# Optimization experiments

Measured on AMD Instinct MI355X. Metric: run time of the kernel, lower is better.

The kernel has to match this reference:

```python
import jax, jax.numpy as jnp
import numpy as np

C = 64        # channel_n
HID = 128     # hidden_size
HEADS = 4
HD = 16       # head_dim = embed_dim // heads, embed_dim overwritten to channel_n
INNER = HEADS * HD  # 64
MLP = 64
H = W = 64    # img_size
B = 8
STEPS = 6
IN_CH = 1     # input_channels
SCALE = HD ** -0.5


def conv3x3_reflect(x, w, b):
    # x: [B,C,H,W], w: [O,I,3,3] -- reflect padding like nn.Conv2d(padding_mode='reflect')
    xp = jnp.pad(x, ((0, 0), (0, 0), (1, 1), (1, 1)), mode='reflect')
    y = jax.lax.conv_general_dilated(xp, w, (1, 1), 'VALID',
                                     dimension_numbers=('NCHW', 'OIHW', 'NCHW'))
    return y + b[None, :, None, None]


def layernorm(x, w, b, axes):
    mu = jnp.mean(x, axis=axes, keepdims=True)
    var = jnp.var(x, axis=axes, keepdims=True)
    return (x - mu) * jax.lax.rsqrt(var + 1e-5) * w + b


def localize(t, h, w):
    # t: [B,heads,n,d] -> [B,heads,n,9,d]; zero-padded 3x3 neighbourhoods
    # (equivalent to grouped conv with 9 unit-impulse filters, padding='same')
    b, nh, n, d = t.shape
    g = t.reshape(b, nh, h, w, d)
    gp = jnp.pad(g, ((0, 0), (0, 0), (1, 1), (1, 1), (0, 0)))
    nb = jnp.stack([gp[:, :, i:i + h, j:j + w, :]
                    for i in range(3) for j in range(3)], axis=4)
    return nb.reshape(b, nh, n, 9, d)


def attn_block(t, ln_w, ln_b, qkv_w, out_w, out_b):
    y = layernorm(t, ln_w, ln_b, -1)
    qkv = y @ qkv_w.T                              # [B,n,3*inner]
    q, k, v = jnp.split(qkv, 3, axis=-1)
    to_heads = lambda z: z.reshape(z.shape[0], z.shape[1], HEADS, HD).transpose(0, 2, 1, 3)
    q, k, v = to_heads(q), to_heads(k), to_heads(v)   # [B,h,n,d]
    kl = localize(k, H, W)                          # [B,h,n,9,d]
    vl = localize(v, H, W)
    dots = jnp.einsum('bhnd,bhnkd->bhnk', q, kl) * SCALE
    a = jax.nn.softmax(dots, axis=-1)               # [B,h,n,9]
    o = jnp.einsum('bhnk,bhnkd->bhnd', a, vl)
    o = o.transpose(0, 2, 1, 3).reshape(t.shape[0], t.shape[1], INNER)
    return o @ out_w.T + out_b


def ff_block(t, ln_w, ln_b, w1, b1, w2, b2):
    y = layernorm(t, ln_w, ln_b, -1)
    y = jax.nn.gelu(y @ w1.T + b1, approximate=False)
    return y @ w2.T + b2


def setup_inputs() -> dict:
    key = jax.random.key(0)
    ks = jax.random.split(key, 20)
    s = 0.02
    inp = {
        'x': jax.random.normal(ks[0], (B, H, W, C), jnp.float32),
        'masks': jax.random.bernoulli(ks[1], 0.5, (STEPS, B, H, W, 1)),
        'p0_w': jax.random.normal(ks[2], (C, C, 3, 3)) * s,
        'p0_b': jnp.zeros((C,)),
        'p1_w': jax.random.normal(ks[3], (C, C, 3, 3)) * s,
        'p1_b': jnp.zeros((C,)),
        'fc0_w': jax.random.normal(ks[4], (HID, 3 * C)) * s,
        'fc0_b': jnp.zeros((HID,)),
        'fc1_w': jax.random.normal(ks[5], (C, HID)) * s,  # zero-init in torch; random here for a non-trivial test
        'norm0_w': jnp.ones((H, W, HID)),
        'norm0_b': jnp.zeros((H, W, HID)),
        'ln1_w': jnp.ones((C,)),
        'ln1_b': jnp.zeros((C,)),
        'qkv_w': jax.random.normal(ks[6], (3 * INNER, C)) * s,
        'out_w': jax.random.normal(ks[7], (C, INNER)) * s,
        'out_b': jnp.zeros((C,)),
        'ln2_w': jnp.ones((C,)),
        'ln2_b': jnp.zeros((C,)),
        'ff1_w': jax.random.normal(ks[8], (MLP, C)) * s,
        'ff1_b': jnp.zeros((MLP,)),
        'ff2_w': jax.random.normal(ks[9], (C, MLP)) * s,
        'ff2_b': jnp.zeros((C,)),
        'steps': STEPS,
    }
    return inp


def reference(x, masks, p0_w, p0_b, p1_w, p1_b, fc0_w, fc0_b, fc1_w,
              norm0_w, norm0_b, ln1_w, ln1_b, qkv_w, out_w, out_b,
              ln2_w, ln2_b, ff1_w, ff1_b, ff2_w, ff2_b, steps):
    def step(xc, mask):
        # ---- NCA perception + update (BackboneNCA.perceive + fc0/relu/norm/fc1) ----
        xt = xc.transpose(0, 3, 1, 2)                      # [B,C,H,W]
        y1 = conv3x3_reflect(xt, p0_w, p0_b)
        y2 = conv3x3_reflect(xt, p1_w, p1_b)
        p = jnp.concatenate([xt, y1, y2], 1).transpose(0, 2, 3, 1)  # [B,H,W,3C]
        hd = jax.nn.relu(p @ fc0_w.T + fc0_b)              # [B,H,W,HID]
        hd = layernorm(hd, norm0_w, norm0_b, (-3, -2, -1))  # norm0 over [H,W,HID]
        dx = hd @ fc1_w.T                                   # [B,H,W,C]
        dx = dx * mask.astype(xc.dtype)                     # stochastic fire
        xn = xc + dx
        # ---- ViT block with localized (3x3 windowed) attention ----
        t = xn.reshape(B, H * W, C)
        t = t + attn_block(t, ln1_w, ln1_b, qkv_w, out_w, out_b)
        t = t + ff_block(t, ln2_w, ln2_b, ff1_w, ff1_b, ff2_w, ff2_b)
        xn = t.reshape(B, H, W, C)
        # keep input channels unchanged
        xn = jnp.concatenate([xc[..., :IN_CH], xn[..., IN_CH:]], axis=-1)
        return xn, None

    out, _ = jax.lax.scan(step, x, masks)
    return out
```

## Files before the change

kernel.cpp:

```cpp
#include <hip/hip_runtime.h>
#include <hip/hip_bf16.h>

typedef __hip_bfloat16 bf16;
typedef __attribute__((ext_vector_type(8))) short bf16x8;
typedef __attribute__((ext_vector_type(4))) float f32x4;

#define NSTEP 6

static __device__ __forceinline__ float b2f(bf16 v) { return __bfloat162float(v); }

static __device__ __forceinline__ float ldp(const void* p, int i, int md) {
    return md ? ((const float*)p)[i] : b2f(((const bf16*)p)[i]);
}
static __device__ __forceinline__ float finz(float v) {
    return (v == v && v * 0.0f == 0.0f) ? v : 0.0f;
}
static __device__ __forceinline__ unsigned short f2bfu(float v) {
    bf16 h = __float2bfloat16(v);
    return *(unsigned short*)&h;
}

static __device__ __forceinline__ void ld_bf8(const bf16* p, float* f) {
    union { uint4 u; unsigned short s[8]; } r;
    r.u = *(const uint4*)p;
#pragma unroll
    for (int j = 0; j < 8; ++j) f[j] = __uint_as_float(((unsigned)r.s[j]) << 16);
}
static __device__ __forceinline__ void ldp8(const void* p, int i, int md, float* f) {
    if (md) {
        const float* fp = (const float*)p + i;
        float4 a = *(const float4*)fp, b = *(const float4*)(fp + 4);
        f[0]=a.x; f[1]=a.y; f[2]=a.z; f[3]=a.w; f[4]=b.x; f[5]=b.y; f[6]=b.z; f[7]=b.w;
    } else {
        ld_bf8((const bf16*)p + i, f);
    }
}
static __device__ __forceinline__ uint4 pk_bf8(const float* f) {
    union { uint4 u; unsigned short s[8]; } r;
#pragma unroll
    for (int j = 0; j < 8; ++j) r.s[j] = f2bfu(f[j]);
    return r.u;
}


__global__ void k_detect(const uint4* __restrict__ m4,
                         const uint4* __restrict__ x4,
                         int* __restrict__ flags, float* __restrict__ accv) {
    __shared__ int s3f, sup, slo, sf32;
    int t = threadIdx.x;
    if (t == 0) { s3f = 0; sup = 0; slo = 0; sf32 = 0; }
    if (t < 96) accv[t] = 0.f;
    __syncthreads();
    int l3f = 0, lup = 0, llo = 0, lf = 0;
    for (int i = t; i < 3072; i += 256) {
        uint4 v = m4[i];
        const unsigned* d = (const unsigned*)&v;
#pragma unroll
        for (int j = 0; j < 4; ++j) {
            unsigned w = d[j];
            unsigned x3f = w ^ 0x3F3F3F3Fu;
            if ((x3f - 0x01010101u) & ~x3f & 0x80808080u) l3f = 1;
            if (w & 0xFFFFFF00u) lup = 1;
            if (w & 0x0000FFFFu) llo = 1;
        }
    }
    for (int i = t; i < 4096; i += 256) {
        uint4 v = x4[i];
        const unsigned* d = (const unsigned*)&v;
#pragma unroll
        for (int j = 0; j < 4; ++j) {
            unsigned bb = (d[j] >> 8) & 0x7Fu;
            if (bb > 0x48u) lf = 1;
        }
    }
    if (l3f) atomicOr(&s3f, 1);
    if (lup) atomicOr(&sup, 1);
    if (llo) atomicOr(&slo, 1);
    if (lf)  atomicOr(&sf32, 1);
    __syncthreads();
    if (t == 0) {
        int mode;
        if (!s3f && !sup) mode = 0;
        else if (!s3f)    mode = 1;
        else if (slo)     mode = 2;
        else              mode = 3;
        flags[0] = mode;
        flags[1] = sf32;
    }
}

__global__ void k_cast(const void* __restrict__ in, float* __restrict__ out,
                       const int* __restrict__ mflags, int n8) {
    int md = mflags[1];
    int i = blockIdx.x * 256 + threadIdx.x;
    if (i < n8) {
        float f[8];
        ldp8(in, i * 8, md, f);
#pragma unroll
        for (int j = 0; j < 8; ++j) f[j] = finz(f[j]);
        *(float4*)&out[i * 8]     = make_float4(f[0], f[1], f[2], f[3]);
        *(float4*)&out[i * 8 + 4] = make_float4(f[4], f[5], f[6], f[7]);
    }
}

__global__ void k_pack_multi(const void* __restrict__ pa, const void* __restrict__ pb,
                             const void* __restrict__ pc, const void* __restrict__ pd,
                             const void* __restrict__ pe, const void* __restrict__ pf,
                             short* __restrict__ out, const int* __restrict__ mflags) {
    int md = mflags[1];
    int i = blockIdx.x * 256 + threadIdx.x;
    if (i >= 57344) return;
    float v;
    if      (i < 24576) v = ldp(pa, i, md);
    else if (i < 32768) v = ldp(pb, i - 24576, md);
    else if (i < 45056) v = ldp(pc, i - 32768, md);
    else if (i < 49152) v = ldp(pd, i - 45056, md);
    else if (i < 53248) v = ldp(pe, i - 49152, md);
    else                v = ldp(pf, i - 53248, md);
    out[i] = (short)f2bfu(v);
}

__global__ void k_pack_bt1(const void* __restrict__ p0, const void* __restrict__ p1,
                           short* __restrict__ out, const int* __restrict__ mflags) {
    int md = mflags[1];
    int i = blockIdx.x * 256 + threadIdx.x;
    if (i < 128 * 576) {
        int o = i / 576, k = i % 576;
        int kk = k >> 6, ii = k & 63;
        float v = (o < 64) ? ldp(p0, o * 576 + ii * 9 + kk, md)
                           : ldp(p1, (o - 64) * 576 + ii * 9 + kk, md);
        out[i] = (short)f2bfu(v);
    }
}

__global__ void k_fold(const void* __restrict__ n0w, const void* __restrict__ n0b,
                       const short* __restrict__ fc1s, float* __restrict__ wsum,
                       float* __restrict__ bconst, const int* __restrict__ mflags) {
    __shared__ short fc1T[128 * 64];
    int md = mflags[1];
    int t = threadIdx.x;
    for (int e = t; e < 8192; e += 256) {
        int c2 = e >> 7, j = e & 127;
        fc1T[j * 64 + c2] = fc1s[c2 * 128 + j];
    }
    __syncthreads();
    int c = t & 63, pl = t >> 6;
    int pos = blockIdx.x * 4 + pl;
    float ws = 0.f, bs = 0.f;
    for (int j = 0; j < 128; ++j) {
        float f = b2f(*(const bf16*)&fc1T[j * 64 + c]);
        ws = fmaf(ldp(n0w, pos * 128 + j, md), f, ws);
        bs = fmaf(ldp(n0b, pos * 128 + j, md), f, bs);
    }
    wsum[pos * 64 + c]   = ws;
    bconst[pos * 64 + c] = bs;
}


__global__ __launch_bounds__(512) void k_perceive(
    const float* __restrict__ xin, const short* __restrict__ bt1,
    const short* __restrict__ fc0s, const short* __restrict__ fc1s,
    const void* __restrict__ p0b, const void* __restrict__ p1b,
    const void* __restrict__ fc0b, const void* __restrict__ n0w,
    const int* __restrict__ mflags, float* __restrict__ t1,
    float* __restrict__ accv, int step)
{
    __shared__ __align__(16) short xpad_s[3 * 66 * 72];
    __shared__ __align__(16) short P_s[64 * 200];
    __shared__ __align__(16) short hd_s[64 * 136];
    __shared__ float red[32];
    int md = mflags[1];
    int bh = blockIdx.x;
    int b = bh >> 6, h = bh & 63;
    int t = threadIdx.x;

    for (int e = t; e < 1536; e += 512) {
        int c8 = e & 7, w = (e >> 3) & 63, r = e >> 9;
        int hr = h - 1 + r; hr = hr < 0 ? -hr : (hr > 63 ? 126 - hr : hr);
        const float* src = xin + ((((b << 6) + hr) << 6) | w) * 64 + c8 * 8;
        float f[8];
        float4 v0 = *(const float4*)src, v1 = *(const float4*)(src + 4);
        f[0]=v0.x; f[1]=v0.y; f[2]=v0.z; f[3]=v0.w; f[4]=v1.x; f[5]=v1.y; f[6]=v1.z; f[7]=v1.w;
        uint4 pv = pk_bf8(f);
        *(uint4*)&xpad_s[((r * 66) + w + 1) * 72 + c8 * 8] = pv;
        if (r == 1) *(uint4*)&P_s[w * 200 + c8 * 8] = pv;
    }
    if (t < 48) {
        int c8 = t & 7, side = (t >> 3) & 1, r = t >> 4;
        int hr = h - 1 + r; hr = hr < 0 ? -hr : (hr > 63 ? 126 - hr : hr);
        int wsrc = side ? 62 : 1, wp = side ? 65 : 0;
        const float* src = xin + ((((b << 6) + hr) << 6) | wsrc) * 64 + c8 * 8;
        float f[8];
        float4 v0 = *(const float4*)src, v1 = *(const float4*)(src + 4);
        f[0]=v0.x; f[1]=v0.y; f[2]=v0.z; f[3]=v0.w; f[4]=v1.x; f[5]=v1.y; f[6]=v1.z; f[7]=v1.w;
        *(uint4*)&xpad_s[((r * 66) + wp) * 72 + c8 * 8] = pk_bf8(f);
    }
    __syncthreads();

    int og  = __builtin_amdgcn_readfirstlane(t >> 6);
    int l   = t & 63, nl = l & 15, q = l >> 4;
    int mt0 = (og & 1) * 2;
    int nt0 = (og >> 1) * 2;
    int o0  = nt0 * 16 + nl, o1 = o0 + 16;

    f32x4 acc[2][2];
#pragma unroll
    for (int i = 0; i < 2; ++i)
#pragma unroll
        for (int j = 0; j < 2; ++j) acc[i][j] = (f32x4){0.f, 0.f, 0.f, 0.f};

    for (int kt = 0; kt < 18; ++kt) {
        int kk = kt >> 1, c0 = (kt & 1) << 5;
        int r = kk / 3, cxi = kk - r * 3;
        bf16x8 b0 = *(const bf16x8*)(bt1 + o0 * 576 + kt * 32 + q * 8);
        bf16x8 b1 = *(const bf16x8*)(bt1 + o1 * 576 + kt * 32 + q * 8);
        bf16x8 a0 = *(const bf16x8*)&xpad_s[((r * 66) + mt0 * 16 + nl + cxi) * 72 + c0 + q * 8];
        bf16x8 a1 = *(const bf16x8*)&xpad_s[((r * 66) + mt0 * 16 + 16 + nl + cxi) * 72 + c0 + q * 8];
        acc[0][0] = __builtin_amdgcn_mfma_f32_16x16x32_bf16(a0, b0, acc[0][0], 0, 0, 0);
        acc[0][1] = __builtin_amdgcn_mfma_f32_16x16x32_bf16(a0, b1, acc[0][1], 0, 0, 0);
        acc[1][0] = __builtin_amdgcn_mfma_f32_16x16x32_bf16(a1, b0, acc[1][0], 0, 0, 0);
        acc[1][1] = __builtin_amdgcn_mfma_f32_16x16x32_bf16(a1, b1, acc[1][1], 0, 0, 0);
    }
    {
        float bias0 = (o0 < 64) ? ldp(p0b, o0, md) : ldp(p1b, o0 - 64, md);
        float bias1 = (o1 < 64) ? ldp(p0b, o1, md) : ldp(p1b, o1 - 64, md);
#pragma unroll
        for (int i = 0; i < 2; ++i)
#pragma unroll
            for (int j = 0; j < 2; ++j) {
                int oo = j ? o1 : o0;
                float bb = j ? bias1 : bias0;
#pragma unroll
                for (int r2 = 0; r2 < 4; ++r2) {
                    int m = (mt0 + i) * 16 + q * 4 + r2;
                    P_s[m * 200 + 64 + oo] = (short)f2bfu(acc[i][j][r2] + bb);
                }
            }
    }
    __syncthreads();

#pragma unroll
    for (int i = 0; i < 2; ++i)
#pragma unroll
        for (int j = 0; j < 2; ++j) acc[i][j] = (f32x4){0.f, 0.f, 0.f, 0.f};
    for (int kt = 0; kt < 6; ++kt) {
        bf16x8 b0 = *(const bf16x8*)(fc0s + o0 * 192 + kt * 32 + q * 8);
        bf16x8 b1 = *(const bf16x8*)(fc0s + o1 * 192 + kt * 32 + q * 8);
        bf16x8 a0 = *(const bf16x8*)&P_s[(mt0 * 16 + nl) * 200 + kt * 32 + q * 8];
        bf16x8 a1 = *(const bf16x8*)&P_s[(mt0 * 16 + 16 + nl) * 200 + kt * 32 + q * 8];
        acc[0][0] = __builtin_amdgcn_mfma_f32_16x16x32_bf16(a0, b0, acc[0][0], 0, 0, 0);
        acc[0][1] = __builtin_amdgcn_mfma_f32_16x16x32_bf16(a0, b1, acc[0][1], 0, 0, 0);
        acc[1][0] = __builtin_amdgcn_mfma_f32_16x16x32_bf16(a1, b0, acc[1][0], 0, 0, 0);
        acc[1][1] = __builtin_amdgcn_mfma_f32_16x16x32_bf16(a1, b1, acc[1][1], 0, 0, 0);
    }
    float lsum = 0.f, lsq = 0.f;
    {
        float fb0 = ldp(fc0b, o0, md), fb1 = ldp(fc0b, o1, md);
#pragma unroll
        for (int i = 0; i < 2; ++i)
#pragma unroll
            for (int j = 0; j < 2; ++j) {
                int oo = j ? o1 : o0;
                float bb = j ? fb1 : fb0;
#pragma unroll
                for (int r2 = 0; r2 < 4; ++r2) {
                    int m = (mt0 + i) * 16 + q * 4 + r2;
                    float v = fmaxf(acc[i][j][r2] + bb, 0.f);
                    unsigned short hu = f2bfu(v);
                    hd_s[m * 136 + oo] = (short)hu;
                    float vr = __uint_as_float(((unsigned)hu) << 16);
                    lsum += vr; lsq += vr * vr;
                }
            }
    }
#pragma unroll
    for (int off = 32; off > 0; off >>= 1) {
        lsum += __shfl_down(lsum, off, 64);
        lsq  += __shfl_down(lsq,  off, 64);
    }
    if (l == 0) { red[og] = lsum; red[16 + og] = lsq; }
    __syncthreads();
    if (t == 0) {
        float a = 0.f, s2 = 0.f;
#pragma unroll
        for (int w = 0; w < 8; ++w) { a += red[w]; s2 += red[16 + w]; }
        atomicAdd(&accv[step * 16 + b * 2],     a);
        atomicAdd(&accv[step * 16 + b * 2 + 1], s2);
    }

    for (int e = t; e < 1024; e += 512) {
        int pos = e >> 4, j8 = (e & 15) * 8;
        float hv[8], wv[8];
        ld_bf8((const bf16*)&hd_s[pos * 136 + j8], hv);
        ldp8(n0w, (h * 64 + pos) * 128 + j8, md, wv);
#pragma unroll
        for (int j = 0; j < 8; ++j) hv[j] *= wv[j];
        *(uint4*)&hd_s[pos * 136 + j8] = pk_bf8(hv);
    }
    __syncthreads();

    {
        int mt = og & 3, nh = og >> 2;
        int to0 = nh * 32 + nl, to1 = to0 + 16;
        f32x4 a0 = (f32x4){0.f,0.f,0.f,0.f}, a1 = (f32x4){0.f,0.f,0.f,0.f};
#pragma unroll
        for (int kt = 0; kt < 4; ++kt) {
            bf16x8 av = *(const bf16x8*)&hd_s[(mt * 16 + nl) * 136 + kt * 32 + q * 8];
            bf16x8 b0 = *(const bf16x8*)(fc1s + to0 * 128 + kt * 32 + q * 8);
            bf16x8 b1 = *(const bf16x8*)(fc1s + to1 * 128 + kt * 32 + q * 8);
            a0 = __builtin_amdgcn_mfma_f32_16x16x32_bf16(av, b0, a0, 0, 0, 0);
            a1 = __builtin_amdgcn_mfma_f32_16x16x32_bf16(av, b1, a1, 0, 0, 0);
        }
#pragma unroll
        for (int r2 = 0; r2 < 4; ++r2) {
            int m = mt * 16 + q * 4 + r2;
            t1[((bh << 6) + m) * 64 + to0] = a0[r2];
            t1[((bh << 6) + m) * 64 + to1] = a1[r2];
        }
    }
}

__global__ __launch_bounds__(512) void k_step2(
    const float* __restrict__ xin, float* __restrict__ xout,
    const float* __restrict__ t1, const float* __restrict__ wsum,
    const float* __restrict__ bconst, const void* __restrict__ mraw,
    const short* __restrict__ qkvs, const void* __restrict__ ln1w,
    const void* __restrict__ ln1b, const short* __restrict__ outs,
    const short* __restrict__ ff1s, const short* __restrict__ ff2s,
    const void* __restrict__ outb, const void* __restrict__ ln2w,
    const void* __restrict__ ln2b, const void* __restrict__ ff1b,
    const void* __restrict__ ff2b, const int* __restrict__ mflags,
    const float* __restrict__ accv, void* __restrict__ dout,
    int step, int write_out)
{
    __shared__ __align__(16) char smraw[75456];
    short* Ks = (short*)smraw;
    short* Vs = (short*)(smraw + 28512);
    short* qo = (short*)(smraw + 57024);
    short* ys = (short*)(smraw + 66240);
    short* Ao = (short*)smraw;
    float* ts = (float*)(smraw + 9216);
    short* hs = (short*)(smraw + 25856);

    int md = mflags[1];
    int bh = blockIdx.x;
    int b = bh >> 6, h = bh & 63;
    int t = threadIdx.x;

    const float invN = 1.f / 524288.f;
    float mean = accv[step * 16 + b * 2] * invN;
    float var  = accv[step * 16 + b * 2 + 1] * invN - mean * mean;
    float rstd = rsqrtf(fmaxf(var, 0.f) + 1e-5f);
    float mrs  = mean * rstd;

    if (t < 96) {
        int kind = (t >= 48) ? 1 : 0, u = t - kind * 48;
        int r = u >> 4, side = (u >> 3) & 1, c8 = u & 7;
        short* dst = kind ? Vs : Ks;
        uint4 z = {0, 0, 0, 0};
        *(uint4*)&dst[((r * 66) + (side ? 65 : 0)) * 72 + c8 * 8] = z;
    }

    int og = __builtin_amdgcn_readfirstlane(t >> 6);
    int l = t & 63, nl = l & 15, q = l >> 4;
    int tok = t >> 3, j8 = (t & 7) * 8;
    int mmode = mflags[0];

    float tn[8];
    float c0 = 0.f;
#pragma unroll
    for (int ci = 0; ci < 8; ++ci) tn[ci] = 0.f;

    for (int r = 0; r < 3; ++r) {
        int hr = h - 1 + r;
        __syncthreads();
        if (hr < 0 || hr > 63) {
            for (int e = t; e < 1024; e += 512) {
                int kind = (e >= 512) ? 1 : 0, u = e & 511;
                int w = u >> 3, c8 = u & 7;
                short* dst = kind ? Vs : Ks;
                uint4 z = {0, 0, 0, 0};
                *(uint4*)&dst[((r * 66) + w + 1) * 72 + c8 * 8] = z;
            }
            continue;
        }
        {
            int row = (b * 64 + hr) * 64 + tok;
            int ppos = hr * 64 + tok;
            const float* xr = xin + row * 64 + j8;
            float4 x0 = *(const float4*)xr, x1 = *(const float4*)(xr + 4);
            float xv[8] = {x0.x, x0.y, x0.z, x0.w, x1.x, x1.y, x1.z, x1.w};
            const float* t1r = t1 + row * 64 + j8;
            float4 a0 = *(const float4*)t1r, a1 = *(const float4*)(t1r + 4);
            float tv[8] = {a0.x, a0.y, a0.z, a0.w, a1.x, a1.y, a1.z, a1.w};
            const float* wr = wsum + ppos * 64 + j8;
            float4 w0 = *(const float4*)wr, w1 = *(const float4*)(wr + 4);
            float wv[8] = {w0.x, w0.y, w0.z, w0.w, w1.x, w1.y, w1.z, w1.w};
            const float* br = bconst + ppos * 64 + j8;
            float4 b0 = *(const float4*)br, b1 = *(const float4*)(br + 4);
            float bc[8] = {b0.x, b0.y, b0.z, b0.w, b1.x, b1.y, b1.z, b1.w};

            int midx = ((step * 8 + b) * 64 + hr) * 64 + tok;
            int mk;
            if (mmode == 0)      mk = ((const int*)mraw)[midx] != 0;
            else if (mmode == 1) mk = ((const unsigned char*)mraw)[midx] != 0;
            else if (mmode == 2) mk = ((const unsigned short*)mraw)[midx] != 0;
            else                 mk = ((const float*)mraw)[midx] != 0.0f;

            float vloc[8];
            float ls = 0.f, lq = 0.f;
#pragma unroll
            for (int ci = 0; ci < 8; ++ci) {
                float dx = rstd * tv[ci] - mrs * wv[ci] + bc[ci];
                vloc[ci] = finz(mk ? (xv[ci] + dx) : xv[ci]);
                ls += vloc[ci]; lq += vloc[ci] * vloc[ci];
            }
            if (r == 1) {
#pragma unroll
                for (int ci = 0; ci < 8; ++ci) tn[ci] = vloc[ci];
                if (j8 == 0) c0 = xv[0];
            }
#pragma unroll
            for (int off = 1; off < 8; off <<= 1) {
                ls += __shfl_xor(ls, off, 64);
                lq += __shfl_xor(lq, off, 64);
            }
            float mu = ls * (1.f / 64.f);
            float vr = lq * (1.f / 64.f) - mu * mu;
            float rs = rsqrtf(fmaxf(vr, 0.f) + 1e-5f);
            float lw[8], lb[8];
            ldp8(ln1w, j8, md, lw);
            ldp8(ln1b, j8, md, lb);
            float yv[8];
#pragma unroll
            for (int ci = 0; ci < 8; ++ci)
                yv[ci] = (vloc[ci] - mu) * rs * lw[ci] + lb[ci];
            *(uint4*)&ys[tok * 72 + j8] = pk_bf8(yv);
        }
        __syncthreads();
        {
            int mt = og & 3, nh2 = og >> 2;
            f32x4 qa[6];
#pragma unroll
            for (int n = 0; n < 6; ++n) qa[n] = (f32x4){0.f, 0.f, 0.f, 0.f};
#pragma unroll
            for (int kt = 0; kt < 2; ++kt) {
                bf16x8 av = *(const bf16x8*)&ys[(mt * 16 + nl) * 72 + kt * 32 + q * 8];
#pragma unroll
                for (int n = 0; n < 6; ++n) {
                    bf16x8 bv = *(const bf16x8*)(qkvs + (((nh2 * 6 + n) * 16) + nl) * 64 + kt * 32 + q * 8);
                    qa[n] = __builtin_amdgcn_mfma_f32_16x16x32_bf16(av, bv, qa[n], 0, 0, 0);
                }
            }
#pragma unroll
            for (int n = 0; n < 6; ++n) {
                int nt = nh2 * 6 + n;
#pragma unroll
                for (int r2 = 0; r2 < 4; ++r2) {
                    int m = mt * 16 + q * 4 + r2;
                    short hv = (short)f2bfu(qa[n][r2]);
                    if (nt < 4) { if (r == 1) qo[m * 72 + nt * 16 + nl] = hv; }
                    else if (nt < 8) Ks[((r * 66) + m + 1) * 72 + (nt - 4) * 16 + nl] = hv;
                    else             Vs[((r * 66) + m + 1) * 72 + (nt - 8) * 16 + nl] = hv;
                }
            }
        }
    }
    __syncthreads();

    int head = __builtin_amdgcn_readfirstlane(t >> 6) & 3;
    int pos  = t & 63;
    bool act = t < 256;
    float o[16];
    if (act) {
        float qv[16];
        ld_bf8((const bf16*)&qo[pos * 72 + head * 16], qv);
        ld_bf8((const bf16*)&qo[pos * 72 + head * 16 + 8], qv + 8);

        float a9[9];
#pragma unroll
        for (int r = 0; r < 3; ++r)
#pragma unroll
            for (int cxi = 0; cxi < 3; ++cxi) {
                const short* kp = &Ks[((r * 66) + pos + cxi) * 72 + head * 16];
                float kf[16];
                ld_bf8((const bf16*)kp, kf);
                ld_bf8((const bf16*)(kp + 8), kf + 8);
                float dot = 0.f;
#pragma unroll
                for (int d = 0; d < 16; ++d) dot = fmaf(qv[d], kf[d], dot);
                a9[r * 3 + cxi] = dot * 0.25f;
            }
        float mx = a9[0];
#pragma unroll
        for (int k = 1; k < 9; ++k) mx = fmaxf(mx, a9[k]);
        float ssum = 0.f;
#pragma unroll
        for (int k = 0; k < 9; ++k) { a9[k] = __expf(a9[k] - mx); ssum += a9[k]; }
        float inv = 1.f / ssum;
#pragma unroll
        for (int k = 0; k < 9; ++k) a9[k] *= inv;

#pragma unroll
        for (int d = 0; d < 16; ++d) o[d] = 0.f;
#pragma unroll
        for (int r = 0; r < 3; ++r)
#pragma unroll
            for (int cxi = 0; cxi < 3; ++cxi) {
                const short* vp = &Vs[((r * 66) + pos + cxi) * 72 + head * 16];
                float vf[16];
                ld_bf8((const bf16*)vp, vf);
                ld_bf8((const bf16*)(vp + 8), vf + 8);
                float w = a9[r * 3 + cxi];
#pragma unroll
                for (int d = 0; d < 16; ++d) o[d] = fmaf(w, vf[d], o[d]);
            }
    }
    __syncthreads();
    if (act) {
        *(uint4*)&Ao[pos * 72 + head * 16]     = pk_bf8(o);
        *(uint4*)&Ao[pos * 72 + head * 16 + 8] = pk_bf8(o + 8);
    }
    __syncthreads();

    int mt = og & 3;
    int nt0 = (og >> 2) * 2;
    int o0 = nt0 * 16 + nl, o1 = o0 + 16;

    {
        f32x4 pa[2];
        pa[0] = (f32x4){0.f,0.f,0.f,0.f}; pa[1] = (f32x4){0.f,0.f,0.f,0.f};
#pragma unroll
        for (int kt = 0; kt < 2; ++kt) {
            bf16x8 av = *(const bf16x8*)&Ao[(mt * 16 + nl) * 72 + kt * 32 + q * 8];
            bf16x8 b0 = *(const bf16x8*)(outs + o0 * 64 + kt * 32 + q * 8);
            bf16x8 b1 = *(const bf16x8*)(outs + o1 * 64 + kt * 32 + q * 8);
            pa[0] = __builtin_amdgcn_mfma_f32_16x16x32_bf16(av, b0, pa[0], 0, 0, 0);
            pa[1] = __builtin_amdgcn_mfma_f32_16x16x32_bf16(av, b1, pa[1], 0, 0, 0);
        }
        float ob0 = ldp(outb, o0, md), ob1 = ldp(outb, o1, md);
#pragma unroll
        for (int j = 0; j < 2; ++j)
#pragma unroll
            for (int r2 = 0; r2 < 4; ++r2) {
                int m = mt * 16 + q * 4 + r2;
                ts[m * 65 + (j ? o1 : o0)] = pa[j][r2] + (j ? ob1 : ob0);
            }
    }
    __syncthreads();

    {
        float v[8];
        float ls = 0.f, lq = 0.f;
#pragma unroll
        for (int ci = 0; ci < 8; ++ci) {
            v[ci] = ts[tok * 65 + j8 + ci] + tn[ci];
            ts[tok * 65 + j8 + ci] = v[ci];
            ls += v[ci]; lq += v[ci] * v[ci];
        }
#pragma unroll
        for (int off = 1; off < 8; off <<= 1) {
            ls += __shfl_xor(ls, off, 64);
            lq += __shfl_xor(lq, off, 64);
        }
        float mu = ls * (1.f / 64.f);
        float vr = lq * (1.f / 64.f) - mu * mu;
        float rs = rsqrtf(fmaxf(vr, 0.f) + 1e-5f);
        float wv[8], bv[8];
        ldp8(ln2w, j8, md, wv);
        ldp8(ln2b, j8, md, bv);
        float yv[8];
#pragma unroll
        for (int ci = 0; ci < 8; ++ci) yv[ci] = (v[ci] - mu) * rs * wv[ci] + bv[ci];
        *(uint4*)&ys[tok * 72 + j8] = pk_bf8(yv);
    }
    __syncthreads();

    {
        f32x4 ma[2];
        ma[0] = (f32x4){0.f,0.f,0.f,0.f}; ma[1] = (f32x4){0.f,0.f,0.f,0.f};
#pragma unroll
        for (int kt = 0; kt < 2; ++kt) {
            bf16x8 av = *(const bf16x8*)&ys[(mt * 16 + nl) * 72 + kt * 32 + q * 8];
            bf16x8 b0 = *(const bf16x8*)(ff1s + o0 * 64 + kt * 32 + q * 8);
            bf16x8 b1 = *(const bf16x8*)(ff1s + o1 * 64 + kt * 32 + q * 8);
            ma[0] = __builtin_amdgcn_mfma_f32_16x16x32_bf16(av, b0, ma[0], 0, 0, 0);
            ma[1] = __builtin_amdgcn_mfma_f32_16x16x32_bf16(av, b1, ma[1], 0, 0, 0);
        }
        float f1b0 = ldp(ff1b, o0, md), f1b1 = ldp(ff1b, o1, md);
#pragma unroll
        for (int j = 0; j < 2; ++j)
#pragma unroll
            for (int r2 = 0; r2 < 4; ++r2) {
                int m = mt * 16 + q * 4 + r2;
                float v = ma[j][r2] + (j ? f1b1 : f1b0);
                float g = 0.5f * v * (1.f + erff(v * 0.70710678118654752f));
                hs[m * 72 + (j ? o1 : o0)] = (short)f2bfu(g);
            }
    }
    __syncthreads();

    {
        f32x4 fa[2];
        fa[0] = (f32x4){0.f,0.f,0.f,0.f}; fa[1] = (f32x4){0.f,0.f,0.f,0.f};
#pragma unroll
        for (int kt = 0; kt < 2; ++kt) {
            bf16x8 av = *(const bf16x8*)&hs[(mt * 16 + nl) * 72 + kt * 32 + q * 8];
            bf16x8 b0 = *(const bf16x8*)(ff2s + o0 * 64 + kt * 32 + q * 8);
            bf16x8 b1 = *(const bf16x8*)(ff2s + o1 * 64 + kt * 32 + q * 8);
            fa[0] = __builtin_amdgcn_mfma_f32_16x16x32_bf16(av, b0, fa[0], 0, 0, 0);
            fa[1] = __builtin_amdgcn_mfma_f32_16x16x32_bf16(av, b1, fa[1], 0, 0, 0);
        }
        float f2b0 = ldp(ff2b, o0, md), f2b1 = ldp(ff2b, o1, md);
#pragma unroll
        for (int j = 0; j < 2; ++j)
#pragma unroll
            for (int r2 = 0; r2 < 4; ++r2) {
                int m = mt * 16 + q * 4 + r2;
                int oo = j ? o1 : o0;
                ts[m * 65 + oo] += fa[j][r2] + (j ? f2b1 : f2b0);
            }
    }
    __syncthreads();

    {
        int idx = ((bh << 6) + tok) * 64 + j8;
        float fv[8];
#pragma unroll
        for (int ci = 0; ci < 8; ++ci) {
            float v = ts[tok * 65 + j8 + ci];
            if (j8 == 0 && ci == 0) v = c0;
            fv[ci] = finz(v);
        }
        *(float4*)&xout[idx]     = make_float4(fv[0], fv[1], fv[2], fv[3]);
        *(float4*)&xout[idx + 4] = make_float4(fv[4], fv[5], fv[6], fv[7]);
        if (write_out) {
            if (md) {
                *(float4*)&((float*)dout)[idx]     = make_float4(fv[0], fv[1], fv[2], fv[3]);
                *(float4*)&((float*)dout)[idx + 4] = make_float4(fv[4], fv[5], fv[6], fv[7]);
            } else {
                *(uint4*)&((bf16*)dout)[idx] = pk_bf8(fv);
            }
        }
    }
}


extern "C" void kernel_launch(void* const* d_in, const int* in_sizes, int n_in,
                              void* d_out, int out_size, void* d_ws, size_t ws_size,
                              hipStream_t stream) {
    (void)in_sizes; (void)n_in; (void)out_size; (void)ws_size;
    const void* x     = d_in[0];
    const void* masks = d_in[1];
    const void* p0w   = d_in[2];
    const void* p0b   = d_in[3];
    const void* p1w   = d_in[4];
    const void* p1b   = d_in[5];
    const void* fc0w  = d_in[6];
    const void* fc0b  = d_in[7];
    const void* fc1w  = d_in[8];
    const void* n0w   = d_in[9];
    const void* n0b   = d_in[10];
    const void* ln1w  = d_in[11];
    const void* ln1b  = d_in[12];
    const void* qkvw  = d_in[13];
    const void* outw  = d_in[14];
    const void* outb  = d_in[15];
    const void* ln2w  = d_in[16];
    const void* ln2b  = d_in[17];
    const void* ff1w  = d_in[18];
    const void* ff1b  = d_in[19];
    const void* ff2w  = d_in[20];
    const void* ff2b  = d_in[21];

    char* wsb = (char*)d_ws;
    float* xst0   = (float*)(wsb + 0);
    float* xst1   = (float*)(wsb + 8388608);
    float* t1buf  = (float*)(wsb + 16777216);
    short* bt1    = (short*)(wsb + 25165824);
    short* packs  = (short*)(wsb + 25313280);
    float* wsumb  = (float*)(wsb + 25427968);
    float* bconb  = (float*)(wsb + 26476544);
    float* accv   = (float*)(wsb + 27525120);
    int*   mflags = (int*)  (wsb + 27525504);

    short* fc0s = packs;
    short* fc1s = packs + 24576;
    short* qkvs = packs + 32768;
    short* outs = packs + 45056;
    short* ff1s = packs + 49152;
    short* ff2s = packs + 53248;

    k_detect<<<1, 256, 0, stream>>>((const uint4*)masks, (const uint4*)x, mflags, accv);
    k_cast<<<1024, 256, 0, stream>>>(x, xst0, mflags, 262144);
    k_pack_bt1<<<288, 256, 0, stream>>>(p0w, p1w, bt1, mflags);
    k_pack_multi<<<224, 256, 0, stream>>>(fc0w, fc1w, qkvw, outw, ff1w, ff2w, packs, mflags);
    k_fold<<<1024, 256, 0, stream>>>(n0w, n0b, fc1s, wsumb, bconb, mflags);

    float* xbuf[2] = {xst0, xst1};
    for (int s = 0; s < NSTEP; ++s) {
        float* cur = xbuf[s & 1];
        float* nxt = xbuf[(s + 1) & 1];
        k_perceive<<<512, 512, 0, stream>>>(cur, bt1, fc0s, fc1s, p0b, p1b, fc0b,
                                            n0w, mflags, t1buf, accv, s);
        k_step2<<<512, 512, 0, stream>>>(cur, nxt, t1buf, wsumb, bconb, masks,
                                         qkvs, ln1w, ln1b, outs, ff1s, ff2s,
                                         outb, ln2w, ln2b, ff1b, ff2b, mflags,
                                         accv, d_out, s, (s == NSTEP - 1) ? 1 : 0);
    }
}
```

Measured before the change: 628.4 us.

## Split step kernel to compute QKV once per row instead of thrice

The fused step kernel recomputed the NCA update, LayerNorm and QKV projection for three image rows per block to get the 3x3 halo, which tripled that work. The step now has two kernels. The first computes the updated state and QKV once per row and writes QKV to a bf16 workspace buffer. The second loads neighbouring K/V rows from global memory, then runs attention and the feed-forward block. This trades redundant compute for an extra launch per step and extra global traffic for the QKV buffer.

```diff
diff --git a/kernel.cpp b/kernel.cpp
--- a/kernel.cpp
+++ b/kernel.cpp
@@ -320,38 +320,140 @@
     }
 }
 
-__global__ __launch_bounds__(512) void k_step2(
-    const float* __restrict__ xin, float* __restrict__ xout,
+__global__ __launch_bounds__(512) void k_upd(
+    const float* __restrict__ xin, float* __restrict__ xnew,
     const float* __restrict__ t1, const float* __restrict__ wsum,
     const float* __restrict__ bconst, const void* __restrict__ mraw,
     const short* __restrict__ qkvs, const void* __restrict__ ln1w,
-    const void* __restrict__ ln1b, const short* __restrict__ outs,
-    const short* __restrict__ ff1s, const short* __restrict__ ff2s,
-    const void* __restrict__ outb, const void* __restrict__ ln2w,
-    const void* __restrict__ ln2b, const void* __restrict__ ff1b,
-    const void* __restrict__ ff2b, const int* __restrict__ mflags,
-    const float* __restrict__ accv, void* __restrict__ dout,
-    int step, int write_out)
+    const void* __restrict__ ln1b, const int* __restrict__ mflags,
+    const float* __restrict__ accv, bf16* __restrict__ qkv, int step)
 {
-    __shared__ __align__(16) char smraw[75456];
-    short* Ks = (short*)smraw;
-    short* Vs = (short*)(smraw + 28512);
-    short* qo = (short*)(smraw + 57024);
-    short* ys = (short*)(smraw + 66240);
-    short* Ao = (short*)smraw;
-    float* ts = (float*)(smraw + 9216);
-    short* hs = (short*)(smraw + 25856);
-
+    __shared__ __align__(16) short ys[64 * 72];
+    __shared__ __align__(16) short qo[64 * 200];
     int md = mflags[1];
     int bh = blockIdx.x;
     int b = bh >> 6, h = bh & 63;
     int t = threadIdx.x;
-
     const float invN = 1.f / 524288.f;
     float mean = accv[step * 16 + b * 2] * invN;
     float var  = accv[step * 16 + b * 2 + 1] * invN - mean * mean;
     float rstd = rsqrtf(fmaxf(var, 0.f) + 1e-5f);
     float mrs  = mean * rstd;
+
+    int tok = t >> 3, j8 = (t & 7) * 8;
+    int idx = ((bh << 6) + tok) * 64 + j8;
+    int ppos = (h * 64 + tok) * 64 + j8;
+    {
+        float4 x0 = *(const float4*)&xin[idx], x1 = *(const float4*)&xin[idx + 4];
+        float xv[8] = {x0.x, x0.y, x0.z, x0.w, x1.x, x1.y, x1.z, x1.w};
+        float4 a0 = *(const float4*)&t1[idx], a1 = *(const float4*)&t1[idx + 4];
+        float tv[8] = {a0.x, a0.y, a0.z, a0.w, a1.x, a1.y, a1.z, a1.w};
+        float4 w0 = *(const float4*)&wsum[ppos], w1 = *(const float4*)&wsum[ppos + 4];
+        float wv[8] = {w0.x, w0.y, w0.z, w0.w, w1.x, w1.y, w1.z, w1.w};
+        float4 b0 = *(const float4*)&bconst[ppos], b1 = *(const float4*)&bconst[ppos + 4];
+        float bc[8] = {b0.x, b0.y, b0.z, b0.w, b1.x, b1.y, b1.z, b1.w};
+
+        int mmode = mflags[0];
+        int midx = ((step * 8 + b) * 64 + h) * 64 + tok;
+        int mk;
+        if (mmode == 0)      mk = ((const int*)mraw)[midx] != 0;
+        else if (mmode == 1) mk = ((const unsigned char*)mraw)[midx] != 0;
+        else if (mmode == 2) mk = ((const unsigned short*)mraw)[midx] != 0;
+        else                 mk = ((const float*)mraw)[midx] != 0.0f;
+
+        float vloc[8];
+        float ls = 0.f, lq = 0.f;
+#pragma unroll
+        for (int ci = 0; ci < 8; ++ci) {
+            float dx = rstd * tv[ci] - mrs * wv[ci] + bc[ci];
+            vloc[ci] = finz(mk ? (xv[ci] + dx) : xv[ci]);
+            ls += vloc[ci]; lq += vloc[ci] * vloc[ci];
+        }
+        *(float4*)&xnew[idx]     = make_float4(vloc[0], vloc[1], vloc[2], vloc[3]);
+        *(float4*)&xnew[idx + 4] = make_float4(vloc[4], vloc[5], vloc[6], vloc[7]);
+#pragma unroll
+        for (int off = 1; off < 8; off <<= 1) {
+            ls += __shfl_xor(ls, off, 64);
+            lq += __shfl_xor(lq, off, 64);
+        }
+        float mu = ls * (1.f / 64.f);
+        float vr = lq * (1.f / 64.f) - mu * mu;
+        float rs = rsqrtf(fmaxf(vr, 0.f) + 1e-5f);
+        float lw[8], lb[8];
+        ldp8(ln1w, j8, md, lw);
+        ldp8(ln1b, j8, md, lb);
+        float yv[8];
+#pragma unroll
+        for (int ci = 0; ci < 8; ++ci)
+            yv[ci] = (vloc[ci] - mu) * rs * lw[ci] + lb[ci];
+        *(uint4*)&ys[tok * 72 + j8] = pk_bf8(yv);
+    }
+    __syncthreads();
+
+    int og = __builtin_amdgcn_readfirstlane(t >> 6);
+    int l = t & 63, nl = l & 15, q = l >> 4;
+    {
+        int mt = og & 3, nh2 = og >> 2;
+        f32x4 qa[6];
+#pragma unroll
+        for (int n = 0; n < 6; ++n) qa[n] = (f32x4){0.f, 0.f, 0.f, 0.f};
+#pragma unroll
+        for (int kt = 0; kt < 2; ++kt) {
+            bf16x8 av = *(const bf16x8*)&ys[(mt * 16 + nl) * 72 + kt * 32 + q * 8];
+#pragma unroll
+            for (int n = 0; n < 6; ++n) {
+                bf16x8 bv = *(const bf16x8*)(qkvs + (((nh2 * 6 + n) * 16) + nl) * 64 + kt * 32 + q * 8);
+                qa[n] = __builtin_amdgcn_mfma_f32_16x16x32_bf16(av, bv, qa[n], 0, 0, 0);
+            }
+        }
+#pragma unroll
+        for (int n = 0; n < 6; ++n)
+#pragma unroll
+            for (int r2 = 0; r2 < 4; ++r2) {
+                int m = mt * 16 + q * 4 + r2;
+                qo[m * 200 + (nh2 * 6 + n) * 16 + nl] = (short)f2bfu(qa[n][r2]);
+            }
+    }
+    __syncthreads();
+
+    for (int e = t; e < 1536; e += 512) {
+        int p2 = e / 24, c8 = e - p2 * 24;
+        *(uint4*)(qkv + ((bh << 6) + p2) * 192 + c8 * 8) =
+            *(const uint4*)&qo[p2 * 200 + c8 * 8];
+    }
+}
+
+__global__ __launch_bounds__(512) void k_attn_ff(
+    const bf16* __restrict__ qkv, const float* __restrict__ xold,
+    float* __restrict__ xnew, const short* __restrict__ outs,
+    const short* __restrict__ ff1s, const short* __restrict__ ff2s,
+    const void* __restrict__ outb, const void* __restrict__ ln2w,
+    const void* __restrict__ ln2b, const void* __restrict__ ff1b,
+    const void* __restrict__ ff2b, const int* __restrict__ mflags,
+    void* __restrict__ dout, int write_out)
+{
+    __shared__ __align__(16) char smraw[66240];
+    short* Ks = (short*)smraw;
+    short* Vs = (short*)(smraw + 28512);
+    short* Ao = (short*)(smraw + 57024);
+    float* ts = (float*)smraw;
+    short* ys = (short*)(smraw + 16640);
+    short* hs = (short*)(smraw + 25856);
+
+    int md = mflags[1];
+    int bh = blockIdx.x;
+    int b = bh >> 6, h = bh & 63;
+    int t = threadIdx.x;
+    int tok = t >> 3, j8 = (t & 7) * 8;
+    int idx = ((bh << 6) + tok) * 64 + j8;
+
+    float xn8[8];
+    {
+        float4 x0 = *(const float4*)&xnew[idx], x1 = *(const float4*)&xnew[idx + 4];
+        xn8[0]=x0.x; xn8[1]=x0.y; xn8[2]=x0.z; xn8[3]=x0.w;
+        xn8[4]=x1.x; xn8[5]=x1.y; xn8[6]=x1.z; xn8[7]=x1.w;
+    }
+    float c0 = (j8 == 0) ? xold[idx] : 0.f;
 
     if (t < 96) {
         int kind = (t >= 48) ? 1 : 0, u = t - kind * 48;
@@ -360,122 +462,25 @@
         uint4 z = {0, 0, 0, 0};
         *(uint4*)&dst[((r * 66) + (side ? 65 : 0)) * 72 + c8 * 8] = z;
     }
-
-    int og = __builtin_amdgcn_readfirstlane(t >> 6);
-    int l = t & 63, nl = l & 15, q = l >> 4;
-    int tok = t >> 3, j8 = (t & 7) * 8;
-    int mmode = mflags[0];
-
-    float tn[8];
-    float c0 = 0.f;
-#pragma unroll
-    for (int ci = 0; ci < 8; ++ci) tn[ci] = 0.f;
-
-    for (int r = 0; r < 3; ++r) {
+    for (int e = t; e < 3072; e += 512) {
+        int kind = (e >= 1536) ? 1 : 0, u = e - kind * 1536;
+        int c8 = u & 7, w = (u >> 3) & 63, r = u >> 9;
         int hr = h - 1 + r;
-        __syncthreads();
-        if (hr < 0 || hr > 63) {
-            for (int e = t; e < 1024; e += 512) {
-                int kind = (e >= 512) ? 1 : 0, u = e & 511;
-                int w = u >> 3, c8 = u & 7;
-                short* dst = kind ? Vs : Ks;
-                uint4 z = {0, 0, 0, 0};
-                *(uint4*)&dst[((r * 66) + w + 1) * 72 + c8 * 8] = z;
-            }
-            continue;
-        }
-        {
-            int row = (b * 64 + hr) * 64 + tok;
-            int ppos = hr * 64 + tok;
-            const float* xr = xin + row * 64 + j8;
-            float4 x0 = *(const float4*)xr, x1 = *(const float4*)(xr + 4);
-            float xv[8] = {x0.x, x0.y, x0.z, x0.w, x1.x, x1.y, x1.z, x1.w};
-            const float* t1r = t1 + row * 64 + j8;
-            float4 a0 = *(const float4*)t1r, a1 = *(const float4*)(t1r + 4);
-            float tv[8] = {a0.x, a0.y, a0.z, a0.w, a1.x, a1.y, a1.z, a1.w};
-            const float* wr = wsum + ppos * 64 + j8;
-            float4 w0 = *(const float4*)wr, w1 = *(const float4*)(wr + 4);
-            float wv[8] = {w0.x, w0.y, w0.z, w0.w, w1.x, w1.y, w1.z, w1.w};
-            const float* br = bconst + ppos * 64 + j8;
-            float4 b0 = *(const float4*)br, b1 = *(const float4*)(br + 4);
-            float bc[8] = {b0.x, b0.y, b0.z, b0.w, b1.x, b1.y, b1.z, b1.w};
-
-            int midx = ((step * 8 + b) * 64 + hr) * 64 + tok;
-            int mk;
-            if (mmode == 0)      mk = ((const int*)mraw)[midx] != 0;
-            else if (mmode == 1) mk = ((const unsigned char*)mraw)[midx] != 0;
-            else if (mmode == 2) mk = ((const unsigned short*)mraw)[midx] != 0;
-            else                 mk = ((const float*)mraw)[midx] != 0.0f;
-
-            float vloc[8];
-            float ls = 0.f, lq = 0.f;
-#pragma unroll
-            for (int ci = 0; ci < 8; ++ci) {
-                float dx = rstd * tv[ci] - mrs * wv[ci] + bc[ci];
-                vloc[ci] = finz(mk ? (xv[ci] + dx) : xv[ci]);
-                ls += vloc[ci]; lq += vloc[ci] * vloc[ci];
-            }
-            if (r == 1) {
-#pragma unroll
-                for (int ci = 0; ci < 8; ++ci) tn[ci] = vloc[ci];
-                if (j8 == 0) c0 = xv[0];
-            }
-#pragma unroll
-            for (int off = 1; off < 8; off <<= 1) {
-                ls += __shfl_xor(ls, off, 64);
-                lq += __shfl_xor(lq, off, 64);
-            }
-            float mu = ls * (1.f / 64.f);
-            float vr = lq * (1.f / 64.f) - mu * mu;
-            float rs = rsqrtf(fmaxf(vr, 0.f) + 1e-5f);
-            float lw[8], lb[8];
-            ldp8(ln1w, j8, md, lw);
-            ldp8(ln1b, j8, md, lb);
-            float yv[8];
-#pragma unroll
-            for (int ci = 0; ci < 8; ++ci)
-                yv[ci] = (vloc[ci] - mu) * rs * lw[ci] + lb[ci];
-            *(uint4*)&ys[tok * 72 + j8] = pk_bf8(yv);
-        }
-        __syncthreads();
-        {
-            int mt = og & 3, nh2 = og >> 2;
-            f32x4 qa[6];
-#pragma unroll
-            for (int n = 0; n < 6; ++n) qa[n] = (f32x4){0.f, 0.f, 0.f, 0.f};
-#pragma unroll
-            for (int kt = 0; kt < 2; ++kt) {
-                bf16x8 av = *(const bf16x8*)&ys[(mt * 16 + nl) * 72 + kt * 32 + q * 8];
-#pragma unroll
-                for (int n = 0; n < 6; ++n) {
-                    bf16x8 bv = *(const bf16x8*)(qkvs + (((nh2 * 6 + n) * 16) + nl) * 64 + kt * 32 + q * 8);
-                    qa[n] = __builtin_amdgcn_mfma_f32_16x16x32_bf16(av, bv, qa[n], 0, 0, 0);
-                }
-            }
-#pragma unroll
-            for (int n = 0; n < 6; ++n) {
-                int nt = nh2 * 6 + n;
-#pragma unroll
-                for (int r2 = 0; r2 < 4; ++r2) {
-                    int m = mt * 16 + q * 4 + r2;
-                    short hv = (short)f2bfu(qa[n][r2]);
-                    if (nt < 4) { if (r == 1) qo[m * 72 + nt * 16 + nl] = hv; }
-                    else if (nt < 8) Ks[((r * 66) + m + 1) * 72 + (nt - 4) * 16 + nl] = hv;
-                    else             Vs[((r * 66) + m + 1) * 72 + (nt - 8) * 16 + nl] = hv;
-                }
-            }
-        }
+        uint4 v = {0, 0, 0, 0};
+        if (hr >= 0 && hr <= 63)
+            v = *(const uint4*)(qkv + ((b * 64 + hr) * 64 + w) * 192 + 64 + kind * 64 + c8 * 8);
+        short* dst = kind ? Vs : Ks;
+        *(uint4*)&dst[((r * 66) + w + 1) * 72 + c8 * 8] = v;
     }
     __syncthreads();
 
     int head = __builtin_amdgcn_readfirstlane(t >> 6) & 3;
     int pos  = t & 63;
     bool act = t < 256;
-    float o[16];
     if (act) {
         float qv[16];
-        ld_bf8((const bf16*)&qo[pos * 72 + head * 16], qv);
-        ld_bf8((const bf16*)&qo[pos * 72 + head * 16 + 8], qv + 8);
+        const bf16* qr = qkv + (((b * 64 + h) * 64) + pos) * 192 + head * 16;
+        ld_bf8(qr, qv); ld_bf8(qr + 8, qv + 8);
 
         float a9[9];
 #pragma unroll
@@ -501,6 +506,7 @@
 #pragma unroll
         for (int k = 0; k < 9; ++k) a9[k] *= inv;
 
+        float o[16];
 #pragma unroll
         for (int d = 0; d < 16; ++d) o[d] = 0.f;
 #pragma unroll
@@ -515,14 +521,13 @@
 #pragma unroll
                 for (int d = 0; d < 16; ++d) o[d] = fmaf(w, vf[d], o[d]);
             }
-    }
-    __syncthreads();
-    if (act) {
         *(uint4*)&Ao[pos * 72 + head * 16]     = pk_bf8(o);
         *(uint4*)&Ao[pos * 72 + head * 16 + 8] = pk_bf8(o + 8);
     }
     __syncthreads();
 
+    int og = __builtin_amdgcn_readfirstlane(t >> 6);
+    int l = t & 63, nl = l & 15, qd = l >> 4;
     int mt = og & 3;
     int nt0 = (og >> 2) * 2;
     int o0 = nt0 * 16 + nl, o1 = o0 + 16;
@@ -532,9 +537,9 @@
         pa[0] = (f32x4){0.f,0.f,0.f,0.f}; pa[1] = (f32x4){0.f,0.f,0.f,0.f};
 #pragma unroll
         for (int kt = 0; kt < 2; ++kt) {
-            bf16x8 av = *(const bf16x8*)&Ao[(mt * 16 + nl) * 72 + kt * 32 + q * 8];
-            bf16x8 b0 = *(const bf16x8*)(outs + o0 * 64 + kt * 32 + q * 8);
-            bf16x8 b1 = *(const bf16x8*)(outs + o1 * 64 + kt * 32 + q * 8);
+            bf16x8 av = *(const bf16x8*)&Ao[(mt * 16 + nl) * 72 + kt * 32 + qd * 8];
+            bf16x8 b0 = *(const bf16x8*)(outs + o0 * 64 + kt * 32 + qd * 8);
+            bf16x8 b1 = *(const bf16x8*)(outs + o1 * 64 + kt * 32 + qd * 8);
             pa[0] = __builtin_amdgcn_mfma_f32_16x16x32_bf16(av, b0, pa[0], 0, 0, 0);
             pa[1] = __builtin_amdgcn_mfma_f32_16x16x32_bf16(av, b1, pa[1], 0, 0, 0);
         }
@@ -543,7 +548,7 @@
         for (int j = 0; j < 2; ++j)
 #pragma unroll
             for (int r2 = 0; r2 < 4; ++r2) {
-                int m = mt * 16 + q * 4 + r2;
+                int m = mt * 16 + qd * 4 + r2;
                 ts[m * 65 + (j ? o1 : o0)] = pa[j][r2] + (j ? ob1 : ob0);
             }
     }
@@ -554,7 +559,7 @@
         float ls = 0.f, lq = 0.f;
 #pragma unroll
         for (int ci = 0; ci < 8; ++ci) {
-            v[ci] = ts[tok * 65 + j8 + ci] + tn[ci];
+            v[ci] = ts[tok * 65 + j8 + ci] + xn8[ci];
             ts[tok * 65 + j8 + ci] = v[ci];
             ls += v[ci]; lq += v[ci] * v[ci];
         }
@@ -581,9 +586,9 @@
         ma[0] = (f32x4){0.f,0.f,0.f,0.f}; ma[1] = (f32x4){0.f,0.f,0.f,0.f};
 #pragma unroll
         for (int kt = 0; kt < 2; ++kt) {
-            bf16x8 av = *(const bf16x8*)&ys[(mt * 16 + nl) * 72 + kt * 32 + q * 8];
-            bf16x8 b0 = *(const bf16x8*)(ff1s + o0 * 64 + kt * 32 + q * 8);
-            bf16x8 b1 = *(const bf16x8*)(ff1s + o1 * 64 + kt * 32 + q * 8);
+            bf16x8 av = *(const bf16x8*)&ys[(mt * 16 + nl) * 72 + kt * 32 + qd * 8];
+            bf16x8 b0 = *(const bf16x8*)(ff1s + o0 * 64 + kt * 32 + qd * 8);
+            bf16x8 b1 = *(const bf16x8*)(ff1s + o1 * 64 + kt * 32 + qd * 8);
             ma[0] = __builtin_amdgcn_mfma_f32_16x16x32_bf16(av, b0, ma[0], 0, 0, 0);
             ma[1] = __builtin_amdgcn_mfma_f32_16x16x32_bf16(av, b1, ma[1], 0, 0, 0);
         }
@@ -592,7 +597,7 @@
         for (int j = 0; j < 2; ++j)
 #pragma unroll
             for (int r2 = 0; r2 < 4; ++r2) {
-                int m = mt * 16 + q * 4 + r2;
+                int m = mt * 16 + qd * 4 + r2;
                 float v = ma[j][r2] + (j ? f1b1 : f1b0);
                 float g = 0.5f * v * (1.f + erff(v * 0.70710678118654752f));
                 hs[m * 72 + (j ? o1 : o0)] = (short)f2bfu(g);
@@ -605,9 +610,9 @@
         fa[0] = (f32x4){0.f,0.f,0.f,0.f}; fa[1] = (f32x4){0.f,0.f,0.f,0.f};
 #pragma unroll
         for (int kt = 0; kt < 2; ++kt) {
-            bf16x8 av = *(const bf16x8*)&hs[(mt * 16 + nl) * 72 + kt * 32 + q * 8];
-            bf16x8 b0 = *(const bf16x8*)(ff2s + o0 * 64 + kt * 32 + q * 8);
-            bf16x8 b1 = *(const bf16x8*)(ff2s + o1 * 64 + kt * 32 + q * 8);
+            bf16x8 av = *(const bf16x8*)&hs[(mt * 16 + nl) * 72 + kt * 32 + qd * 8];
+            bf16x8 b0 = *(const bf16x8*)(ff2s + o0 * 64 + kt * 32 + qd * 8);
+            bf16x8 b1 = *(const bf16x8*)(ff2s + o1 * 64 + kt * 32 + qd * 8);
             fa[0] = __builtin_amdgcn_mfma_f32_16x16x32_bf16(av, b0, fa[0], 0, 0, 0);
             fa[1] = __builtin_amdgcn_mfma_f32_16x16x32_bf16(av, b1, fa[1], 0, 0, 0);
         }
@@ -616,7 +621,7 @@
         for (int j = 0; j < 2; ++j)
 #pragma unroll
             for (int r2 = 0; r2 < 4; ++r2) {
-                int m = mt * 16 + q * 4 + r2;
+                int m = mt * 16 + qd * 4 + r2;
                 int oo = j ? o1 : o0;
                 ts[m * 65 + oo] += fa[j][r2] + (j ? f2b1 : f2b0);
             }
@@ -624,7 +629,6 @@
     __syncthreads();
 
     {
-        int idx = ((bh << 6) + tok) * 64 + j8;
         float fv[8];
 #pragma unroll
         for (int ci = 0; ci < 8; ++ci) {
@@ -632,8 +636,8 @@
             if (j8 == 0 && ci == 0) v = c0;
             fv[ci] = finz(v);
         }
-        *(float4*)&xout[idx]     = make_float4(fv[0], fv[1], fv[2], fv[3]);
-        *(float4*)&xout[idx + 4] = make_float4(fv[4], fv[5], fv[6], fv[7]);
+        *(float4*)&xnew[idx]     = make_float4(fv[0], fv[1], fv[2], fv[3]);
+        *(float4*)&xnew[idx + 4] = make_float4(fv[4], fv[5], fv[6], fv[7]);
         if (write_out) {
             if (md) {
                 *(float4*)&((float*)dout)[idx]     = make_float4(fv[0], fv[1], fv[2], fv[3]);
@@ -677,12 +681,13 @@
     float* xst0   = (float*)(wsb + 0);
     float* xst1   = (float*)(wsb + 8388608);
     float* t1buf  = (float*)(wsb + 16777216);
-    short* bt1    = (short*)(wsb + 25165824);
-    short* packs  = (short*)(wsb + 25313280);
-    float* wsumb  = (float*)(wsb + 25427968);
-    float* bconb  = (float*)(wsb + 26476544);
-    float* accv   = (float*)(wsb + 27525120);
-    int*   mflags = (int*)  (wsb + 27525504);
+    bf16*  qkvb   = (bf16*) (wsb + 25165824);
+    short* bt1    = (short*)(wsb + 37748736);
+    short* packs  = (short*)(wsb + 37896192);
+    float* wsumb  = (float*)(wsb + 38010880);
+    float* bconb  = (float*)(wsb + 39059456);
+    float* accv   = (float*)(wsb + 40108032);
+    int*   mflags = (int*)  (wsb + 40108416);
 
     short* fc0s = packs;
     short* fc1s = packs + 24576;
@@ -703,9 +708,10 @@
         float* nxt = xbuf[(s + 1) & 1];
         k_perceive<<<512, 512, 0, stream>>>(cur, bt1, fc0s, fc1s, p0b, p1b, fc0b,
                                             n0w, mflags, t1buf, accv, s);
-        k_step2<<<512, 512, 0, stream>>>(cur, nxt, t1buf, wsumb, bconb, masks,
-                                         qkvs, ln1w, ln1b, outs, ff1s, ff2s,
-                                         outb, ln2w, ln2b, ff1b, ff2b, mflags,
-                                         accv, d_out, s, (s == NSTEP - 1) ? 1 : 0);
-    }
-}
+        k_upd<<<512, 512, 0, stream>>>(cur, nxt, t1buf, wsumb, bconb, masks,
+                                       qkvs, ln1w, ln1b, mflags, accv, qkvb, s);
+        k_attn_ff<<<512, 512, 0, stream>>>(qkvb, cur, nxt, outs, ff1s, ff2s,
+                                           outb, ln2w, ln2b, ff1b, ff2b, mflags,
+                                           d_out, (s == NSTEP - 1) ? 1 : 0);
+    }
+}
```

After: 577.3 us. -8.1%, faster.
